# Kernel tuning notes

Hardware: AMD Instinct MI355X
Metric: run time of the kernel (lower is better)

## Reference

```python
import jax, jax.numpy as jnp
import numpy as np

N = 200_000      # active voxels
INC = 64
OUTC = 96
GRID = 128
EPS = 1e-5


def _build_neighbor_maps():
    """Precompute gather/scatter index maps for the 26 off-center hypercube
    offsets (the 4th kernel dim has size 1, so offsets live in 3D)."""
    rng = np.random.default_rng(0)
    G = GRID ** 3
    lin = rng.choice(G, size=N, replace=False).astype(np.int64)
    z = lin % GRID
    y = (lin // GRID) % GRID
    x = lin // (GRID * GRID)
    lookup = np.full(G, -1, np.int64)
    lookup[lin] = np.arange(N)
    offsets = [(dx, dy, dz) for dx in (-1, 0, 1) for dy in (-1, 0, 1)
               for dz in (-1, 0, 1) if (dx, dy, dz) != (0, 0, 0)]
    pin, pout = [], []
    for dx, dy, dz in offsets:
        nx, ny, nz = x + dx, y + dy, z + dz
        valid = (nx >= 0) & (nx < GRID) & (ny >= 0) & (ny < GRID) & (nz >= 0) & (nz < GRID)
        nlin = (nx * GRID + ny) * GRID + nz
        nb = np.where(valid, lookup[np.clip(nlin, 0, G - 1)], -1)
        m = nb >= 0
        pin.append(np.arange(N)[m])
        pout.append(nb[m])
    pmax = max(len(p) for p in pin)
    in_idx = np.zeros((26, pmax), np.int64)          # pad gathers row 0 (harmless)
    out_idx = np.full((26, pmax), N, np.int64)       # pad scatters to sink row N
    for k, (pi, po) in enumerate(zip(pin, pout)):
        in_idx[k, : len(pi)] = pi
        out_idx[k, : len(po)] = po
    return in_idx, out_idx


def setup_inputs() -> dict:
    in_idx, out_idx = _build_neighbor_maps()
    key = jax.random.key(0)
    k1, k2, k3 = jax.random.split(key, 3)
    std = 1.0 / np.sqrt(INC * 27)
    feats = jax.random.normal(k1, (N, INC), jnp.float32)
    W_center = jax.random.normal(k2, (INC, OUTC), jnp.float32) * std
    W_off = jax.random.normal(k3, (26, INC, OUTC), jnp.float32) * std
    gamma = jnp.ones((OUTC,), jnp.float32)   # bn.weight init to 1.0
    beta = jnp.zeros((OUTC,), jnp.float32)   # bn.bias init to 0.0
    return {"feats": feats, "W_center": W_center, "W_off": W_off,
            "gamma": gamma, "beta": beta,
            "in_idx": jnp.asarray(in_idx), "out_idx": jnp.asarray(out_idx)}


def reference(feats, W_center, W_off, gamma, beta, in_idx, out_idx):
    # --- sparse conv-transpose: gather -> GEMM -> scatter-add ---
    out = feats @ W_center                                   # center offset: identity map, [N, outc]
    gathered = feats[in_idx]                                 # [26, P, inc]
    contrib = jnp.einsum('kpc,kcd->kpd', gathered, W_off)    # [26, P, outc]
    out = jnp.concatenate([out, jnp.zeros((1, OUTC), out.dtype)], axis=0)  # sink row
    out = out.at[out_idx.reshape(-1)].add(contrib.reshape(-1, OUTC))[:N]
    # --- BatchNorm (training-mode batch stats) + ReLU ---
    mean = out.mean(axis=0)
    var = out.var(axis=0)
    y = (out - mean) * jax.lax.rsqrt(var + EPS) * gamma + beta
    return jax.nn.relu(y)
```

## Files before the change

kernel.cpp:

```cpp
#include <hip/hip_runtime.h>


#define N_VOX   200000
#define INC     64
#define OUTC    96
#define NOFF    26
#define NBLK    782
#define NPAD    200192
#define EPSV    1e-5f

using bf16x8 = __attribute__((ext_vector_type(8))) short;
using u16x8  = __attribute__((ext_vector_type(8))) unsigned short;
using f32x4  = __attribute__((ext_vector_type(4))) float;

__device__ inline unsigned short f2bf(float x) {
    union { float f; unsigned u; } v; v.f = x;
    unsigned r = (v.u + 0x7FFFu + ((v.u >> 16) & 1u)) >> 16;
    return (unsigned short)r;
}

__device__ __forceinline__ void gload_lds16(const void* g, void* l) {
    __builtin_amdgcn_global_load_lds(
        (const __attribute__((address_space(1))) void*)g,
        (__attribute__((address_space(3))) void*)l, 16, 0, 0);
}

__global__ void fill_src_kernel(const int* __restrict__ in_idx,
                                const int* __restrict__ out_idx,
                                int P, int* __restrict__ srcmap) {
    int idx = blockIdx.x * blockDim.x + threadIdx.x;
    if (idx >= NOFF * P) return;
    int dst = out_idx[idx];
    if (dst >= N_VOX) return;
    int k = idx / P;
    srcmap[(size_t)k * NPAD + dst] = in_idx[idx];
}

__global__ void wprep_kernel(const float* __restrict__ Wc,
                             const float* __restrict__ Woff,
                             unsigned short* __restrict__ Wb) {
    int t = blockIdx.x * blockDim.x + threadIdx.x;
    if (t >= 27 * 2 * 6 * 64) return;
    int lane = t & 63;
    int g    = t >> 6;
    int ct   = g % 6;
    int s    = (g / 6) % 2;
    int m    = g / 12;
    const float* W = (m == 26) ? Wc : (Woff + (size_t)m * INC * OUTC);
    int k0 = s * 32 + (lane >> 4) * 8;
    int c  = ct * 16 + (lane & 15);
    bf16x8 v;
    #pragma unroll
    for (int e = 0; e < 8; ++e)
        v[e] = (short)f2bf(W[(size_t)(k0 + e) * OUTC + c]);
    *(bf16x8*)(Wb + (size_t)t * 8) = v;
}

__global__ void fcvt_kernel(const float* __restrict__ feats,
                            unsigned short* __restrict__ featsb) {
    int i = blockIdx.x * blockDim.x + threadIdx.x;
    if (i >= N_VOX * INC / 8) return;
    const float4* src = (const float4*)feats + (size_t)i * 2;
    float4 f0 = src[0], f1 = src[1];
    bf16x8 v;
    v[0] = (short)f2bf(f0.x); v[1] = (short)f2bf(f0.y);
    v[2] = (short)f2bf(f0.z); v[3] = (short)f2bf(f0.w);
    v[4] = (short)f2bf(f1.x); v[5] = (short)f2bf(f1.y);
    v[6] = (short)f2bf(f1.z); v[7] = (short)f2bf(f1.w);
    *(bf16x8*)(featsb + (size_t)i * 8) = v;
}

template<int STAGE_BF16>
__global__ __launch_bounds__(256, 2)
void conv_mfma_kernel(const unsigned short* __restrict__ featsb,
                      const unsigned short* __restrict__ Wb,
                      const int* __restrict__ srcmap,
                      float* __restrict__ outf,
                      unsigned short* __restrict__ stg,
                      float* __restrict__ pstats) {
    __shared__ __align__(16) unsigned short Wlds[2][6144];

    const int t     = threadIdx.x;
    const int wid   = t >> 6;
    const int lane  = t & 63;
    const int blk   = blockIdx.x;
    const int rbase = blk * 256 + wid * 64;
    const int row16 = lane & 15;
    const int kgrp  = lane >> 4;

    f32x4  acc[4][6] = {};
    bf16x8 aC[4][2], aN[4][2];
    int smC[4], smN[4];
    int hasC, hasN;

    #pragma unroll
    for (int i = 0; i < 3; ++i)
        gload_lds16(Wb + (size_t)26 * 6144 + (size_t)(t + 256 * i) * 8,
                    &Wlds[0][(t + 256 * i) * 8]);
    #pragma unroll
    for (int rt = 0; rt < 4; ++rt)
        smC[rt] = srcmap[rbase + rt * 16 + row16];
    #pragma unroll
    for (int rt = 0; rt < 4; ++rt) {
        int row = rbase + rt * 16 + row16;
        int src = row < N_VOX ? row : N_VOX;
        const unsigned short* fr = featsb + (size_t)src * INC + kgrp * 8;
        aC[rt][0] = *(const bf16x8*)fr;
        aC[rt][1] = *(const bf16x8*)(fr + 32);
    }
    hasC = 0xF;
    asm volatile("s_waitcnt vmcnt(0)" ::: "memory");
    __builtin_amdgcn_s_barrier();

    #pragma unroll 2
    for (int idx = 0; idx < 27; ++idx) {
        const int buf = idx & 1;

        if (idx < 26) {
            const unsigned short* wsrc = Wb + (size_t)idx * 6144;
            #pragma unroll
            for (int i = 0; i < 3; ++i)
                gload_lds16(wsrc + (size_t)(t + 256 * i) * 8,
                            &Wlds[buf ^ 1][(t + 256 * i) * 8]);
        }
        asm volatile("" ::: "memory");

        {
            int off = idx + 1; if (off > 25) off = 25;
            #pragma unroll
            for (int rt = 0; rt < 4; ++rt)
                smN[rt] = srcmap[(size_t)off * NPAD + rbase + rt * 16 + row16];
        }
        {
            int h = 0;
            #pragma unroll
            for (int rt = 0; rt < 4; ++rt) {
                if (__ballot(smC[rt] >= 0)) h |= (1 << rt);
                int src = smC[rt] >= 0 ? smC[rt] : N_VOX;
                const unsigned short* fr = featsb + (size_t)src * INC + kgrp * 8;
                aN[rt][0] = *(const bf16x8*)fr;
                aN[rt][1] = *(const bf16x8*)(fr + 32);
            }
            hasN = __builtin_amdgcn_readfirstlane(h);
        }
        asm volatile("" ::: "memory");

        {
            const unsigned short* WL = Wlds[buf];
            #pragma unroll
            for (int ct = 0; ct < 6; ++ct) {
                bf16x8 b0 = *(const bf16x8*)&WL[(size_t)ct * 512 + lane * 8];
                bf16x8 b1 = *(const bf16x8*)&WL[(size_t)(6 + ct) * 512 + lane * 8];
                #pragma unroll
                for (int rt = 0; rt < 4; ++rt) {
                    if (hasC & (1 << rt)) {
                        acc[rt][ct] = __builtin_amdgcn_mfma_f32_16x16x32_bf16(aC[rt][0], b0, acc[rt][ct], 0, 0, 0);
                        acc[rt][ct] = __builtin_amdgcn_mfma_f32_16x16x32_bf16(aC[rt][1], b1, acc[rt][ct], 0, 0, 0);
                    }
                }
            }
        }

        asm volatile("s_waitcnt vmcnt(12)" ::: "memory");
        __builtin_amdgcn_s_barrier();

        #pragma unroll
        for (int rt = 0; rt < 4; ++rt) {
            aC[rt][0] = aN[rt][0]; aC[rt][1] = aN[rt][1]; smC[rt] = smN[rt];
        }
        hasC = hasN;
    }
    __syncthreads();

    float s6[6], q6[6];
    #pragma unroll
    for (int ct = 0; ct < 6; ++ct) {
        float s = 0.f, q = 0.f;
        #pragma unroll
        for (int rt = 0; rt < 4; ++rt) {
            f32x4 a = acc[rt][ct];
            s += a[0] + a[1] + a[2] + a[3];
            q += a[0]*a[0] + a[1]*a[1] + a[2]*a[2] + a[3]*a[3];
        }
        s += __shfl_xor(s, 16); q += __shfl_xor(q, 16);
        s += __shfl_xor(s, 32); q += __shfl_xor(q, 32);
        s6[ct] = s; q6[ct] = q;
    }
    float* sred = (float*)Wlds;
    if (lane < 16) {
        #pragma unroll
        for (int ct = 0; ct < 6; ++ct) {
            sred[wid * 96 + ct * 16 + lane]       = s6[ct];
            sred[384 + wid * 96 + ct * 16 + lane] = q6[ct];
        }
    }
    __syncthreads();
    if (t < 96) {
        float s = sred[t] + sred[96 + t] + sred[192 + t] + sred[288 + t];
        pstats[(size_t)t * NBLK + blk] = s;
    } else if (t < 192) {
        int c = t - 96;
        float q = sred[384 + c] + sred[480 + c] + sred[576 + c] + sred[672 + c];
        pstats[(size_t)(96 + c) * NBLK + blk] = q;
    }

    #pragma unroll
    for (int rt = 0; rt < 4; ++rt) {
        #pragma unroll
        for (int ct = 0; ct < 6; ++ct) {
            #pragma unroll
            for (int j = 0; j < 4; ++j) {
                int row = rbase + rt * 16 + kgrp * 4 + j;
                if (row < N_VOX) {
                    if (STAGE_BF16)
                        stg[(size_t)row * OUTC + ct * 16 + row16] = f2bf(acc[rt][ct][j]);
                    else
                        outf[(size_t)row * OUTC + ct * 16 + row16] = acc[rt][ct][j];
                }
            }
        }
    }
}

__global__ void stats_reduce_kernel(const float* __restrict__ pstats,
                                    const float* __restrict__ gamma,
                                    const float* __restrict__ beta,
                                    float* __restrict__ scsh) {
    int c = blockIdx.x;
    int t = threadIdx.x;
    float s = 0.f, q = 0.f;
    for (int i = t; i < NBLK; i += 256) {
        s += pstats[(size_t)c * NBLK + i];
        q += pstats[(size_t)(96 + c) * NBLK + i];
    }
    #pragma unroll
    for (int d = 1; d < 64; d <<= 1) {
        s += __shfl_xor(s, d);
        q += __shfl_xor(q, d);
    }
    __shared__ float rs[4], rq[4];
    if ((t & 63) == 0) { rs[t >> 6] = s; rq[t >> 6] = q; }
    __syncthreads();
    if (t == 0) {
        s = rs[0] + rs[1] + rs[2] + rs[3];
        q = rq[0] + rq[1] + rq[2] + rq[3];
        float inv_n = 1.0f / (float)N_VOX;
        float mean = s * inv_n;
        float var  = q * inv_n - mean * mean;
        float sc   = gamma[c] * rsqrtf(var + EPSV);
        scsh[c]      = sc;
        scsh[96 + c] = beta[c] - mean * sc;
    }
}

__global__ void apply_bn_bf16_kernel(const unsigned short* __restrict__ stg,
                                     float* __restrict__ out,
                                     const float* __restrict__ scsh) {
    __shared__ float sc[OUTC], sh[OUTC];
    int t = threadIdx.x;
    if (t < OUTC) { sc[t] = scsh[t]; sh[t] = scsh[96 + t]; }
    __syncthreads();
    const int total8 = N_VOX * OUTC / 8;
    for (int i = blockIdx.x * blockDim.x + t; i < total8; i += gridDim.x * blockDim.x) {
        u16x8 v = *(const u16x8*)(stg + (size_t)i * 8);
        int c = (i % 12) * 8;
        float o[8];
        #pragma unroll
        for (int j = 0; j < 8; ++j) {
            union { unsigned u; float f; } w; w.u = (unsigned)v[j] << 16;
            o[j] = fmaxf(fmaf(w.f, sc[c + j], sh[c + j]), 0.f);
        }
        float4* dst = (float4*)(out + (size_t)i * 8);
        dst[0] = make_float4(o[0], o[1], o[2], o[3]);
        dst[1] = make_float4(o[4], o[5], o[6], o[7]);
    }
}

__global__ void apply_bn_fp32_kernel(float* __restrict__ out,
                                     const float* __restrict__ scsh) {
    __shared__ float sc[OUTC], sh[OUTC];
    int t = threadIdx.x;
    if (t < OUTC) { sc[t] = scsh[t]; sh[t] = scsh[96 + t]; }
    __syncthreads();
    const int total4 = N_VOX * OUTC / 4;
    for (int i = blockIdx.x * blockDim.x + t; i < total4; i += gridDim.x * blockDim.x) {
        float4 v = ((float4*)out)[i];
        int c = (i * 4) % OUTC;
        v.x = fmaxf(fmaf(v.x, sc[c    ], sh[c    ]), 0.f);
        v.y = fmaxf(fmaf(v.y, sc[c + 1], sh[c + 1]), 0.f);
        v.z = fmaxf(fmaf(v.z, sc[c + 2], sh[c + 2]), 0.f);
        v.w = fmaxf(fmaf(v.w, sc[c + 3], sh[c + 3]), 0.f);
        ((float4*)out)[i] = v;
    }
}

extern "C" void kernel_launch(void* const* d_in, const int* in_sizes, int n_in,
                              void* d_out, int out_size, void* d_ws, size_t ws_size,
                              hipStream_t stream) {
    const float* feats   = (const float*)d_in[0];
    const float* Wc      = (const float*)d_in[1];
    const float* Woff    = (const float*)d_in[2];
    const float* gamma   = (const float*)d_in[3];
    const float* beta    = (const float*)d_in[4];
    const int*   in_idx  = (const int*)d_in[5];
    const int*   out_idx = (const int*)d_in[6];
    const int P = in_sizes[5] / NOFF;

    char* w = (char*)d_ws;
    int* srcmap = (int*)w;                   w += (size_t)NOFF * NPAD * 4;
    unsigned short* Wb = (unsigned short*)w; w += (size_t)27 * 6144 * 2;
    float* pstats = (float*)w;               w += (size_t)192 * NBLK * 4;
    float* scsh = (float*)w;                 w += 256 * 4;
    unsigned short* featsb = (unsigned short*)w;
    w += (size_t)(N_VOX + 1) * INC * 2;
    unsigned short* stg = (unsigned short*)w;
    size_t need_stg = (size_t)(w - (char*)d_ws) + (size_t)N_VOX * OUTC * 2;
    bool use_stg = (ws_size >= need_stg);

    hipMemsetAsync(srcmap, 0xFF, (size_t)NOFF * NPAD * 4, stream);
    hipMemsetAsync(featsb + (size_t)N_VOX * INC, 0, INC * 2, stream);
    fill_src_kernel<<<(NOFF * P + 255) / 256, 256, 0, stream>>>(in_idx, out_idx, P, srcmap);
    wprep_kernel<<<(27 * 2 * 6 * 64 + 255) / 256, 256, 0, stream>>>(Wc, Woff, Wb);
    fcvt_kernel<<<(N_VOX * INC / 8 + 255) / 256, 256, 0, stream>>>(feats, featsb);

    float* out = (float*)d_out;
    if (use_stg) {
        conv_mfma_kernel<1><<<NBLK, 256, 0, stream>>>(featsb, Wb, srcmap, out, stg, pstats);
        stats_reduce_kernel<<<96, 256, 0, stream>>>(pstats, gamma, beta, scsh);
        apply_bn_bf16_kernel<<<2048, 256, 0, stream>>>(stg, out, scsh);
    } else {
        conv_mfma_kernel<0><<<NBLK, 256, 0, stream>>>(featsb, Wb, srcmap, out, stg, pstats);
        stats_reduce_kernel<<<96, 256, 0, stream>>>(pstats, gamma, beta, scsh);
        apply_bn_fp32_kernel<<<2048, 256, 0, stream>>>(out, scsh);
    }
}
```

Before: 142.7 us.

## Load weight fragments directly from global memory instead of double-buffered LDS staging

Removes the LDS double buffer for per-offset weight tiles along with the global_load_lds prefetch and the per-iteration block barriers. Each wave now reads its B fragments straight from global memory (L2/L1 cached) into registers each offset, and the loop order is swapped to rt-outer. Feature gathers are now predicated so that empty neighbor slots skip the load instead of reading the sink row. This drops synchronisation and LDS traffic, but adds redundant global weight reads across waves, more register pressure, and exposes load latency now that the loop is unroll 1.

```diff
diff --git a/kernel.cpp b/kernel.cpp
--- a/kernel.cpp
+++ b/kernel.cpp
@@ -10,19 +10,12 @@
 #define EPSV    1e-5f
 
 using bf16x8 = __attribute__((ext_vector_type(8))) short;
-using u16x8  = __attribute__((ext_vector_type(8))) unsigned short;
 using f32x4  = __attribute__((ext_vector_type(4))) float;
 
 __device__ inline unsigned short f2bf(float x) {
     union { float f; unsigned u; } v; v.f = x;
     unsigned r = (v.u + 0x7FFFu + ((v.u >> 16) & 1u)) >> 16;
     return (unsigned short)r;
-}
-
-__device__ __forceinline__ void gload_lds16(const void* g, void* l) {
-    __builtin_amdgcn_global_load_lds(
-        (const __attribute__((address_space(1))) void*)g,
-        (__attribute__((address_space(3))) void*)l, 16, 0, 0);
 }
 
 __global__ void fill_src_kernel(const int* __restrict__ in_idx,
@@ -78,7 +71,7 @@
                       float* __restrict__ outf,
                       unsigned short* __restrict__ stg,
                       float* __restrict__ pstats) {
-    __shared__ __align__(16) unsigned short Wlds[2][6144];
+    __shared__ float sred[768];
 
     const int t     = threadIdx.x;
     const int wid   = t >> 6;
@@ -94,10 +87,6 @@
     int hasC, hasN;
 
     #pragma unroll
-    for (int i = 0; i < 3; ++i)
-        gload_lds16(Wb + (size_t)26 * 6144 + (size_t)(t + 256 * i) * 8,
-                    &Wlds[0][(t + 256 * i) * 8]);
-    #pragma unroll
     for (int rt = 0; rt < 4; ++rt)
         smC[rt] = srcmap[rbase + rt * 16 + row16];
     #pragma unroll
@@ -109,68 +98,60 @@
         aC[rt][1] = *(const bf16x8*)(fr + 32);
     }
     hasC = 0xF;
-    asm volatile("s_waitcnt vmcnt(0)" ::: "memory");
-    __builtin_amdgcn_s_barrier();
-
-    #pragma unroll 2
+
+    #pragma unroll 1
     for (int idx = 0; idx < 27; ++idx) {
-        const int buf = idx & 1;
-
-        if (idx < 26) {
-            const unsigned short* wsrc = Wb + (size_t)idx * 6144;
-            #pragma unroll
-            for (int i = 0; i < 3; ++i)
-                gload_lds16(wsrc + (size_t)(t + 256 * i) * 8,
-                            &Wlds[buf ^ 1][(t + 256 * i) * 8]);
-        }
-        asm volatile("" ::: "memory");
-
-        {
-            int off = idx + 1; if (off > 25) off = 25;
+        if (idx < 25) {
             #pragma unroll
             for (int rt = 0; rt < 4; ++rt)
-                smN[rt] = srcmap[(size_t)off * NPAD + rbase + rt * 16 + row16];
-        }
-        {
+                smN[rt] = srcmap[(size_t)(idx + 1) * NPAD + rbase + rt * 16 + row16];
+        }
+
+        if (idx < 26) {
             int h = 0;
             #pragma unroll
             for (int rt = 0; rt < 4; ++rt) {
-                if (__ballot(smC[rt] >= 0)) h |= (1 << rt);
-                int src = smC[rt] >= 0 ? smC[rt] : N_VOX;
-                const unsigned short* fr = featsb + (size_t)src * INC + kgrp * 8;
-                aN[rt][0] = *(const bf16x8*)fr;
-                aN[rt][1] = *(const bf16x8*)(fr + 32);
+                int s = smC[rt];
+                if (__ballot(s >= 0)) h |= (1 << rt);
+                bf16x8 g0 = {}, g1 = {};
+                if (s >= 0) {
+                    const unsigned short* fr = featsb + (size_t)s * INC + kgrp * 8;
+                    g0 = *(const bf16x8*)fr;
+                    g1 = *(const bf16x8*)(fr + 32);
+                }
+                aN[rt][0] = g0; aN[rt][1] = g1;
             }
             hasN = __builtin_amdgcn_readfirstlane(h);
-        }
-        asm volatile("" ::: "memory");
-
-        {
-            const unsigned short* WL = Wlds[buf];
-            #pragma unroll
-            for (int ct = 0; ct < 6; ++ct) {
-                bf16x8 b0 = *(const bf16x8*)&WL[(size_t)ct * 512 + lane * 8];
-                bf16x8 b1 = *(const bf16x8*)&WL[(size_t)(6 + ct) * 512 + lane * 8];
+        } else {
+            hasN = 0;
+        }
+
+        const unsigned short* wb = Wb + (size_t)(idx == 0 ? 26 : idx - 1) * 6144;
+        bf16x8 B0[6], B1[6];
+        #pragma unroll
+        for (int ct = 0; ct < 6; ++ct) {
+            B0[ct] = *(const bf16x8*)(wb + (size_t)ct * 512 + lane * 8);
+            B1[ct] = *(const bf16x8*)(wb + (size_t)(6 + ct) * 512 + lane * 8);
+        }
+
+        #pragma unroll
+        for (int rt = 0; rt < 4; ++rt) {
+            if (hasC & (1 << rt)) {
                 #pragma unroll
-                for (int rt = 0; rt < 4; ++rt) {
-                    if (hasC & (1 << rt)) {
-                        acc[rt][ct] = __builtin_amdgcn_mfma_f32_16x16x32_bf16(aC[rt][0], b0, acc[rt][ct], 0, 0, 0);
-                        acc[rt][ct] = __builtin_amdgcn_mfma_f32_16x16x32_bf16(aC[rt][1], b1, acc[rt][ct], 0, 0, 0);
-                    }
+                for (int ct = 0; ct < 6; ++ct) {
+                    acc[rt][ct] = __builtin_amdgcn_mfma_f32_16x16x32_bf16(aC[rt][0], B0[ct], acc[rt][ct], 0, 0, 0);
+                    acc[rt][ct] = __builtin_amdgcn_mfma_f32_16x16x32_bf16(aC[rt][1], B1[ct], acc[rt][ct], 0, 0, 0);
                 }
             }
         }
 
-        asm volatile("s_waitcnt vmcnt(12)" ::: "memory");
-        __builtin_amdgcn_s_barrier();
-
         #pragma unroll
         for (int rt = 0; rt < 4; ++rt) {
-            aC[rt][0] = aN[rt][0]; aC[rt][1] = aN[rt][1]; smC[rt] = smN[rt];
+            aC[rt][0] = aN[rt][0]; aC[rt][1] = aN[rt][1];
+            smC[rt] = (idx < 25) ? smN[rt] : -1;
         }
         hasC = hasN;
     }
-    __syncthreads();
 
     float s6[6], q6[6];
     #pragma unroll
@@ -186,7 +167,6 @@
         s += __shfl_xor(s, 32); q += __shfl_xor(q, 32);
         s6[ct] = s; q6[ct] = q;
     }
-    float* sred = (float*)Wlds;
     if (lane < 16) {
         #pragma unroll
         for (int ct = 0; ct < 6; ++ct) {
@@ -262,12 +242,12 @@
     __syncthreads();
     const int total8 = N_VOX * OUTC / 8;
     for (int i = blockIdx.x * blockDim.x + t; i < total8; i += gridDim.x * blockDim.x) {
-        u16x8 v = *(const u16x8*)(stg + (size_t)i * 8);
+        bf16x8 v = *(const bf16x8*)(stg + (size_t)i * 8);
         int c = (i % 12) * 8;
         float o[8];
         #pragma unroll
         for (int j = 0; j < 8; ++j) {
-            union { unsigned u; float f; } w; w.u = (unsigned)v[j] << 16;
+            union { unsigned u; float f; } w; w.u = (unsigned)(unsigned short)v[j] << 16;
             o[j] = fmaxf(fmaf(w.f, sc[c + j], sh[c + j]), 0.f);
         }
         float4* dst = (float4*)(out + (size_t)i * 8);
```

Result: no change. 141.5 us (-0.8%).

## Shrink conv block tile to 192 rows and skip gathers for empty neighbor tiles

Applied to the files above, without the earlier changes.

Each block now covers 192 rows (48 per wave) instead of 256, and launch bounds go from 2 to 3 blocks per SM, so more blocks run with fewer registers each. Srcmap indices are loaded once per wave as 48 lanes and spread with shuffles. Feature gathers are skipped for rows with no neighbor, and the MFMA block is skipped per wave when no row has a neighbor. The hand-tuned vmcnt waits and unroll-2 are replaced with plain __syncthreads, which may lose some overlap between the weight prefetch and compute.

```diff
diff --git a/kernel.cpp b/kernel.cpp
--- a/kernel.cpp
+++ b/kernel.cpp
@@ -5,12 +5,12 @@
 #define INC     64
 #define OUTC    96
 #define NOFF    26
-#define NBLK    782
+#define MROWS   192
+#define NBLK    1042
 #define NPAD    200192
 #define EPSV    1e-5f
 
 using bf16x8 = __attribute__((ext_vector_type(8))) short;
-using u16x8  = __attribute__((ext_vector_type(8))) unsigned short;
 using f32x4  = __attribute__((ext_vector_type(4))) float;
 
 __device__ inline unsigned short f2bf(float x) {
@@ -71,7 +71,7 @@
 }
 
 template<int STAGE_BF16>
-__global__ __launch_bounds__(256, 2)
+__global__ __launch_bounds__(256, 3)
 void conv_mfma_kernel(const unsigned short* __restrict__ featsb,
                       const unsigned short* __restrict__ Wb,
                       const int* __restrict__ srcmap,
@@ -84,100 +84,89 @@
     const int wid   = t >> 6;
     const int lane  = t & 63;
     const int blk   = blockIdx.x;
-    const int rbase = blk * 256 + wid * 64;
+    const int rbase = blk * MROWS + wid * 48;
     const int row16 = lane & 15;
     const int kgrp  = lane >> 4;
 
-    f32x4  acc[4][6] = {};
-    bf16x8 aC[4][2], aN[4][2];
-    int smC[4], smN[4];
-    int hasC, hasN;
+    f32x4  acc[3][6] = {};
+    bf16x8 aC[3][2], aN[3][2];
 
     #pragma unroll
     for (int i = 0; i < 3; ++i)
         gload_lds16(Wb + (size_t)26 * 6144 + (size_t)(t + 256 * i) * 8,
                     &Wlds[0][(t + 256 * i) * 8]);
-    #pragma unroll
-    for (int rt = 0; rt < 4; ++rt)
-        smC[rt] = srcmap[rbase + rt * 16 + row16];
-    #pragma unroll
-    for (int rt = 0; rt < 4; ++rt) {
+
+    int sm_next = (lane < 48) ? srcmap[rbase + lane] : -1;
+
+    bool has_cur = false;
+    #pragma unroll
+    for (int rt = 0; rt < 3; ++rt) {
         int row = rbase + rt * 16 + row16;
         int src = row < N_VOX ? row : N_VOX;
         const unsigned short* fr = featsb + (size_t)src * INC + kgrp * 8;
         aC[rt][0] = *(const bf16x8*)fr;
         aC[rt][1] = *(const bf16x8*)(fr + 32);
-    }
-    hasC = 0xF;
-    asm volatile("s_waitcnt vmcnt(0)" ::: "memory");
-    __builtin_amdgcn_s_barrier();
-
-    #pragma unroll 2
+        has_cur = true;
+    }
+    has_cur = __ballot(has_cur) != 0ull;
+    __syncthreads();
+
     for (int idx = 0; idx < 27; ++idx) {
         const int buf = idx & 1;
 
-        if (idx < 26) {
-            const unsigned short* wsrc = Wb + (size_t)idx * 6144;
+        int sm_next2 = -1;
+        if (idx <= 24 && lane < 48)
+            sm_next2 = srcmap[(size_t)(idx + 1) * NPAD + rbase + lane];
+
+        bool has_next = false;
+        if (idx <= 25) {
+            bool any = false;
+            #pragma unroll
+            for (int rt = 0; rt < 3; ++rt) {
+                int src = __shfl(sm_next, rt * 16 + row16);
+                bf16x8 g0 = {}, g1 = {};
+                if (src >= 0) {
+                    const unsigned short* fr = featsb + (size_t)src * INC + kgrp * 8;
+                    g0 = *(const bf16x8*)fr;
+                    g1 = *(const bf16x8*)(fr + 32);
+                    any = true;
+                }
+                aN[rt][0] = g0; aN[rt][1] = g1;
+            }
+            has_next = __ballot(any) != 0ull;
             #pragma unroll
             for (int i = 0; i < 3; ++i)
-                gload_lds16(wsrc + (size_t)(t + 256 * i) * 8,
+                gload_lds16(Wb + (size_t)idx * 6144 + (size_t)(t + 256 * i) * 8,
                             &Wlds[buf ^ 1][(t + 256 * i) * 8]);
         }
-        asm volatile("" ::: "memory");
-
-        {
-            int off = idx + 1; if (off > 25) off = 25;
-            #pragma unroll
-            for (int rt = 0; rt < 4; ++rt)
-                smN[rt] = srcmap[(size_t)off * NPAD + rbase + rt * 16 + row16];
-        }
-        {
-            int h = 0;
-            #pragma unroll
-            for (int rt = 0; rt < 4; ++rt) {
-                if (__ballot(smC[rt] >= 0)) h |= (1 << rt);
-                int src = smC[rt] >= 0 ? smC[rt] : N_VOX;
-                const unsigned short* fr = featsb + (size_t)src * INC + kgrp * 8;
-                aN[rt][0] = *(const bf16x8*)fr;
-                aN[rt][1] = *(const bf16x8*)(fr + 32);
-            }
-            hasN = __builtin_amdgcn_readfirstlane(h);
-        }
-        asm volatile("" ::: "memory");
-
-        {
+
+        if (has_cur) {
             const unsigned short* WL = Wlds[buf];
             #pragma unroll
             for (int ct = 0; ct < 6; ++ct) {
                 bf16x8 b0 = *(const bf16x8*)&WL[(size_t)ct * 512 + lane * 8];
                 bf16x8 b1 = *(const bf16x8*)&WL[(size_t)(6 + ct) * 512 + lane * 8];
                 #pragma unroll
-                for (int rt = 0; rt < 4; ++rt) {
-                    if (hasC & (1 << rt)) {
-                        acc[rt][ct] = __builtin_amdgcn_mfma_f32_16x16x32_bf16(aC[rt][0], b0, acc[rt][ct], 0, 0, 0);
-                        acc[rt][ct] = __builtin_amdgcn_mfma_f32_16x16x32_bf16(aC[rt][1], b1, acc[rt][ct], 0, 0, 0);
-                    }
+                for (int rt = 0; rt < 3; ++rt) {
+                    acc[rt][ct] = __builtin_amdgcn_mfma_f32_16x16x32_bf16(aC[rt][0], b0, acc[rt][ct], 0, 0, 0);
+                    acc[rt][ct] = __builtin_amdgcn_mfma_f32_16x16x32_bf16(aC[rt][1], b1, acc[rt][ct], 0, 0, 0);
                 }
             }
         }
-
-        asm volatile("s_waitcnt vmcnt(12)" ::: "memory");
-        __builtin_amdgcn_s_barrier();
-
-        #pragma unroll
-        for (int rt = 0; rt < 4; ++rt) {
-            aC[rt][0] = aN[rt][0]; aC[rt][1] = aN[rt][1]; smC[rt] = smN[rt];
-        }
-        hasC = hasN;
-    }
-    __syncthreads();
+        __syncthreads();
+
+        #pragma unroll
+        for (int rt = 0; rt < 3; ++rt) { aC[rt][0] = aN[rt][0]; aC[rt][1] = aN[rt][1]; }
+        sm_next = sm_next2;
+        has_cur = has_next;
+    }
 
     float s6[6], q6[6];
     #pragma unroll
     for (int ct = 0; ct < 6; ++ct) {
         float s = 0.f, q = 0.f;
         #pragma unroll
-        for (int rt = 0; rt < 4; ++rt) {
+        for (int rt = 0; rt < 3; ++rt) {
             f32x4 a = acc[rt][ct];
             s += a[0] + a[1] + a[2] + a[3];
             q += a[0]*a[0] + a[1]*a[1] + a[2]*a[2] + a[3]*a[3];
@@ -205,7 +194,7 @@
     }
 
     #pragma unroll
-    for (int rt = 0; rt < 4; ++rt) {
+    for (int rt = 0; rt < 3; ++rt) {
         #pragma unroll
         for (int ct = 0; ct < 6; ++ct) {
             #pragma unroll
@@ -262,12 +251,12 @@
     __syncthreads();
     const int total8 = N_VOX * OUTC / 8;
     for (int i = blockIdx.x * blockDim.x + t; i < total8; i += gridDim.x * blockDim.x) {
-        u16x8 v = *(const u16x8*)(stg + (size_t)i * 8);
+        bf16x8 v = *(const bf16x8*)(stg + (size_t)i * 8);
         int c = (i % 12) * 8;
         float o[8];
         #pragma unroll
         for (int j = 0; j < 8; ++j) {
-            union { unsigned u; float f; } w; w.u = (unsigned)v[j] << 16;
+            union { unsigned u; float f; } w; w.u = (unsigned)(unsigned short)v[j] << 16;
             o[j] = fmaxf(fmaf(w.f, sc[c + j], sh[c + j]), 0.f);
         }
         float4* dst = (float4*)(out + (size_t)i * 8);
```

Result: faster. 119.3 us (-16.4%).
